# Optimization experiments

Measured on AMD Instinct MI355X. Metric: run time of the kernel, lower is better.

## Reference

```python
import jax, jax.numpy as jnp
import numpy as np

N_NODES = 50000
N_EDGES = 800000
HIDDEN = 64
RES = 0.5  # args.res_layer


def setup_inputs() -> dict:
    key = jax.random.key(0)
    ks = jax.random.split(key, 9)
    s = 0.05  # scale weights to keep exp(att) stable
    return {
        "edge_index": jax.random.randint(ks[0], (2, N_EDGES), 0, N_NODES, dtype=jnp.int32),
        "adj_values": jax.random.uniform(ks[1], (N_EDGES,), dtype=jnp.float32),
        "embeds": jax.random.normal(ks[2], (N_NODES, HIDDEN), dtype=jnp.float32),
        "W1": jax.random.normal(ks[3], (HIDDEN, HIDDEN), dtype=jnp.float32) * s,
        "b1": jax.random.normal(ks[4], (HIDDEN,), dtype=jnp.float32) * s,
        "W2": jax.random.normal(ks[5], (HIDDEN, HIDDEN), dtype=jnp.float32) * s,
        "b2": jax.random.normal(ks[6], (HIDDEN,), dtype=jnp.float32) * s,
        "att_w": jax.random.normal(ks[7], (2 * HIDDEN,), dtype=jnp.float32) * s,
        "att_b": jax.random.normal(ks[8], (1,), dtype=jnp.float32) * s,
    }


def reference(edge_index, adj_values, embeds, W1, b1, W2, b2, att_w, att_b):
    n = embeds.shape[0]
    h = embeds.shape[1]
    row, col = edge_index[0], edge_index[1]
    # per-edge gather + two small linears with ReLU
    f1 = jax.nn.relu(embeds[row] @ W1 + b1)          # [E, h]
    f2 = jax.nn.relu(embeds[col] @ W2 + b2)          # [E, h]
    # attention score = Linear(concat(f1, f2)) -> split weight, avoid concat
    att = f1 @ att_w[:h] + f2 @ att_w[h:] + att_b[0]  # [E]
    exp_att = jnp.exp(att)
    # sparse row-wise softmax denominator via segment sum
    rowsum = jax.ops.segment_sum(exp_att, row, num_segments=n) + 1e-6  # [N]
    values = (exp_att / rowsum[row] + RES * adj_values) / (1.0 + RES)  # [E]
    # SpMM: out[i] = sum_{e: row[e]=i} values[e] * embeds[col[e]]
    out = jax.ops.segment_sum(values[:, None] * embeds[col], row, num_segments=n)  # [N, h]
    return values, out
```

## Files before the change

### kernel.cpp

```cpp
#include <hip/hip_runtime.h>
#include <hip/hip_bf16.h>

#define HID 64
#define RES_F 0.5f
#define SLOTS 64

typedef __attribute__((ext_vector_type(8))) short short8;
typedef __attribute__((ext_vector_type(4))) float f32x4;

__device__ __forceinline__ float lane_bcast_f(float v, int k) {
    return __builtin_bit_cast(float, __builtin_amdgcn_readlane(__builtin_bit_cast(int, v), k));
}
__device__ __forceinline__ int lane_bcast_i(int v, int k) {
    return __builtin_amdgcn_readlane(v, k);
}
__device__ __forceinline__ short f2bf(float x) {
    __hip_bfloat16 h = __float2bfloat16(x);
    return __builtin_bit_cast(short, h);
}

__global__ void __launch_bounds__(256) fused_prep_kernel(
    const float* __restrict__ embeds,
    const float* __restrict__ W1, const float* __restrict__ W2,
    const float* __restrict__ b1, const float* __restrict__ b2,
    const float* __restrict__ att_w,
    const int* __restrict__ row, const int* __restrict__ col,
    const float* __restrict__ adj,
    int* __restrict__ cursor, int4* __restrict__ edata,
    float* __restrict__ a1, float* __restrict__ a2,
    __hip_bfloat162* __restrict__ embeds_bf,
    int n, int E, int nodeBlocks, int edgeBlocks)
{
    __shared__ short sW[2 * HID * HID];

    if (blockIdx.x < nodeBlocks) {
        for (int i = threadIdx.x; i < HID * HID; i += blockDim.x) {
            sW[i]             = f2bf(W1[i]);
            sW[HID * HID + i] = f2bf(W2[i]);
        }
        __syncthreads();

        const int lane = threadIdx.x & 63;
        const int colx = lane & 15;
        const int quad = lane >> 4;

        short8 bfrag[8][2];
        float  sac[8], bc[8];
#pragma unroll
        for (int cb = 0; cb < 8; ++cb) {
            const int jp = cb * 16 + colx;
            const short* w = (jp < HID) ? (sW + jp) : (sW + HID * HID + jp - HID);
#pragma unroll
            for (int kh = 0; kh < 2; ++kh) {
                short8 f;
#pragma unroll
                for (int j = 0; j < 8; ++j) {
                    const int k = kh * 32 + quad * 8 + j;
                    f[j] = w[k * HID];
                }
                bfrag[cb][kh] = f;
            }
            sac[cb] = att_w[jp];
            bc[cb]  = (jp < HID) ? b1[jp] : b2[jp - HID];
        }

        int gwave = (blockIdx.x * blockDim.x + threadIdx.x) >> 6;
        const int nwave = (nodeBlocks * blockDim.x) >> 6;
        const int nbatch = (n + 15) >> 4;

        for (int b = gwave; b < nbatch; b += nwave) {
            const int base = b << 4;
            int mrow = base + colx;
            if (mrow >= n) mrow = n - 1;
            const float* ep = embeds + (size_t)mrow * HID;
            short8 afrag0, afrag1;
#pragma unroll
            for (int j = 0; j < 8; ++j) {
                afrag0[j] = f2bf(ep[quad * 8 + j]);
                afrag1[j] = f2bf(ep[32 + quad * 8 + j]);
            }

            float acc1[4] = {0.f, 0.f, 0.f, 0.f};
            float acc2[4] = {0.f, 0.f, 0.f, 0.f};
#pragma unroll
            for (int cb = 0; cb < 8; ++cb) {
                f32x4 C = {0.f, 0.f, 0.f, 0.f};
                C = __builtin_amdgcn_mfma_f32_16x16x32_bf16(afrag0, bfrag[cb][0], C, 0, 0, 0);
                C = __builtin_amdgcn_mfma_f32_16x16x32_bf16(afrag1, bfrag[cb][1], C, 0, 0, 0);
#pragma unroll
                for (int reg = 0; reg < 4; ++reg) {
                    const float v = fmaxf(C[reg] + bc[cb], 0.f) * sac[cb];
                    if (cb < 4) acc1[reg] += v; else acc2[reg] += v;
                }
            }
#pragma unroll
            for (int reg = 0; reg < 4; ++reg) {
#pragma unroll
                for (int off = 1; off < 16; off <<= 1) {
                    acc1[reg] += __shfl_xor(acc1[reg], off, 64);
                    acc2[reg] += __shfl_xor(acc2[reg], off, 64);
                }
            }
            if (colx == 0) {
#pragma unroll
                for (int reg = 0; reg < 4; ++reg) {
                    const int i = base + quad * 4 + reg;
                    if (i < n) { a1[i] = acc1[reg]; a2[i] = acc2[reg]; }
                }
            }
        }
    } else {
        const int tid = (blockIdx.x - nodeBlocks) * blockDim.x + threadIdx.x;
        const int ts  = edgeBlocks * blockDim.x;

        const float2* ef2 = (const float2*)embeds;
        const int npair = n * (HID / 2);
        for (int i = tid; i < npair; i += ts) {
            float2 f = ef2[i];
            __hip_bfloat162 h;
            h.x = __float2bfloat16(f.x);
            h.y = __float2bfloat16(f.y);
            embeds_bf[i] = h;
        }

        for (int e = tid; e < E; e += ts) {
            const int r  = row[e];
            const int c  = col[e];
            const float aj = adj[e];
            const int p  = atomicAdd(&cursor[r], 1);
            if (p < SLOTS)
                edata[(size_t)r * SLOTS + p] =
                    make_int4(c, __float_as_int(aj), e, 0);
        }
    }
}

__global__ void __launch_bounds__(256) spmm_kernel(
    const int* __restrict__ cursor, const int4* __restrict__ edata,
    const __hip_bfloat16* __restrict__ embeds_bf,
    const float* __restrict__ a1, const float* __restrict__ a2,
    const float* __restrict__ att_b,
    float* __restrict__ values, float* __restrict__ out, int n)
{
    const float ab  = att_b[0];
    const float inv = 1.0f / (1.0f + RES_F);
    const int lane = threadIdx.x & 63;
    int r = (blockIdx.x * blockDim.x + threadIdx.x) >> 6;
    const int nwave = (gridDim.x * blockDim.x) >> 6;

    for (; r < n; r += nwave) {
        const int deg = min(cursor[r], SLOTS);
        const float a1r = a1[r];
        float acc = 0.0f;

        const bool valid = lane < deg;
        int c = 0, e = 0;
        float ex = 0.0f, aj = 0.0f;
        if (valid) {
            const int4 ed = edata[(size_t)r * SLOTS + lane];
            c  = ed.x;
            aj = __int_as_float(ed.y);
            e  = ed.z;
            ex = __expf(a1r + a2[c] + ab);
        }
        float rs = ex;
#pragma unroll
        for (int off = 1; off < 64; off <<= 1)
            rs += __shfl_xor(rs, off, 64);
        float v = 0.0f;
        if (valid) {
            v = (ex / (rs + 1e-6f) + RES_F * aj) * inv;
            values[e] = v;
        }
        int j = 0;
        for (; j + 8 <= deg; j += 8) {
            const int   c0 = lane_bcast_i(c, j + 0);
            const int   c1 = lane_bcast_i(c, j + 1);
            const int   c2 = lane_bcast_i(c, j + 2);
            const int   c3 = lane_bcast_i(c, j + 3);
            const int   c4 = lane_bcast_i(c, j + 4);
            const int   c5 = lane_bcast_i(c, j + 5);
            const int   c6 = lane_bcast_i(c, j + 6);
            const int   c7 = lane_bcast_i(c, j + 7);
            const float b0 = __bfloat162float(embeds_bf[c0 * HID + lane]);
            const float b1 = __bfloat162float(embeds_bf[c1 * HID + lane]);
            const float b2 = __bfloat162float(embeds_bf[c2 * HID + lane]);
            const float b3 = __bfloat162float(embeds_bf[c3 * HID + lane]);
            const float b4 = __bfloat162float(embeds_bf[c4 * HID + lane]);
            const float b5 = __bfloat162float(embeds_bf[c5 * HID + lane]);
            const float b6 = __bfloat162float(embeds_bf[c6 * HID + lane]);
            const float b7 = __bfloat162float(embeds_bf[c7 * HID + lane]);
            acc = fmaf(lane_bcast_f(v, j + 0), b0, acc);
            acc = fmaf(lane_bcast_f(v, j + 1), b1, acc);
            acc = fmaf(lane_bcast_f(v, j + 2), b2, acc);
            acc = fmaf(lane_bcast_f(v, j + 3), b3, acc);
            acc = fmaf(lane_bcast_f(v, j + 4), b4, acc);
            acc = fmaf(lane_bcast_f(v, j + 5), b5, acc);
            acc = fmaf(lane_bcast_f(v, j + 6), b6, acc);
            acc = fmaf(lane_bcast_f(v, j + 7), b7, acc);
        }
        for (; j < deg; ++j) {
            const int   cj = lane_bcast_i(c, j);
            const float vj = lane_bcast_f(v, j);
            acc = fmaf(vj, __bfloat162float(embeds_bf[cj * HID + lane]), acc);
        }
        out[r * HID + lane] = acc;
    }
}

extern "C" void kernel_launch(void* const* d_in, const int* in_sizes, int n_in,
                              void* d_out, int out_size, void* d_ws, size_t ws_size,
                              hipStream_t stream)
{
    const int* edge_index = (const int*)d_in[0];
    const float* adj      = (const float*)d_in[1];
    const float* embeds   = (const float*)d_in[2];
    const float* W1       = (const float*)d_in[3];
    const float* b1       = (const float*)d_in[4];
    const float* W2       = (const float*)d_in[5];
    const float* b2       = (const float*)d_in[6];
    const float* att_w    = (const float*)d_in[7];
    const float* att_b    = (const float*)d_in[8];

    const int E = in_sizes[1];
    const int N = in_sizes[2] / HID;

    const int* row = edge_index;
    const int* col = edge_index + E;

    int4*  edata  = (int4*)d_ws;
    float* a1     = (float*)(edata + (size_t)N * SLOTS);
    float* a2     = a1 + N;
    int*   cursor = (int*)(a2 + N);
    __hip_bfloat16* embeds_bf = (__hip_bfloat16*)(cursor + N);

    float* values = (float*)d_out;
    float* out    = values + E;

    (void)hipMemsetAsync(cursor, 0, (size_t)N * sizeof(int), stream);

    const int nodeBlocks = 512;
    const int edgeBlocks = 3125;
    fused_prep_kernel<<<nodeBlocks + edgeBlocks, 256, 0, stream>>>(
        embeds, W1, W2, b1, b2, att_w, row, col, adj,
        cursor, edata, a1, a2, (__hip_bfloat162*)embeds_bf,
        N, E, nodeBlocks, edgeBlocks);

    spmm_kernel<<<12544, 256, 0, stream>>>(cursor, edata, embeds_bf,
                                           a1, a2, att_b, values, out, N);
}
```

Measured before the change: 165.9 us.

## Write edge values to slot layout and remap with separate kernel

The bucket entry shrinks from int4 to int2 by dropping the edge index. The SpMM kernel now writes attention values into a coalesced per-row slot buffer instead of scattering them by edge id. A new remap kernel uses a per-edge recorded slot position to gather the values back into edge order. This replaces scattered writes with coalesced ones, at the cost of an extra kernel launch, an extra pos array write and read, and a gather read of the slot buffer.

```diff
diff --git a/kernel.cpp b/kernel.cpp
--- a/kernel.cpp
+++ b/kernel.cpp
@@ -26,7 +26,8 @@
     const float* __restrict__ att_w,
     const int* __restrict__ row, const int* __restrict__ col,
     const float* __restrict__ adj,
-    int* __restrict__ cursor, int4* __restrict__ edata,
+    int* __restrict__ cursor, int* __restrict__ pos,
+    int2* __restrict__ edata,
     float* __restrict__ a1, float* __restrict__ a2,
     __hip_bfloat162* __restrict__ embeds_bf,
     int n, int E, int nodeBlocks, int edgeBlocks)
@@ -127,20 +128,21 @@
             const int r  = row[e];
             const int c  = col[e];
             const float aj = adj[e];
-            const int p  = atomicAdd(&cursor[r], 1);
+            const int p = atomicAdd(&cursor[r], 1);
+            pos[e] = p;
             if (p < SLOTS)
                 edata[(size_t)r * SLOTS + p] =
-                    make_int4(c, __float_as_int(aj), e, 0);
+                    make_int2(c, __float_as_int(aj));
         }
     }
 }
 
 __global__ void __launch_bounds__(256) spmm_kernel(
-    const int* __restrict__ cursor, const int4* __restrict__ edata,
+    const int* __restrict__ cursor, const int2* __restrict__ edata,
     const __hip_bfloat16* __restrict__ embeds_bf,
     const float* __restrict__ a1, const float* __restrict__ a2,
     const float* __restrict__ att_b,
-    float* __restrict__ values, float* __restrict__ out, int n)
+    float* __restrict__ vslot, float* __restrict__ out, int n)
 {
     const float ab  = att_b[0];
     const float inv = 1.0f / (1.0f + RES_F);
@@ -154,13 +156,12 @@
         float acc = 0.0f;
 
         const bool valid = lane < deg;
-        int c = 0, e = 0;
+        int c = 0;
         float ex = 0.0f, aj = 0.0f;
         if (valid) {
-            const int4 ed = edata[(size_t)r * SLOTS + lane];
+            const int2 ed = edata[(size_t)r * SLOTS + lane];
             c  = ed.x;
             aj = __int_as_float(ed.y);
-            e  = ed.z;
             ex = __expf(a1r + a2[c] + ab);
         }
         float rs = ex;
@@ -170,7 +171,7 @@
         float v = 0.0f;
         if (valid) {
             v = (ex / (rs + 1e-6f) + RES_F * aj) * inv;
-            values[e] = v;
+            vslot[(size_t)r * SLOTS + lane] = v;
         }
         int j = 0;
         for (; j + 8 <= deg; j += 8) {
@@ -208,6 +209,20 @@
     }
 }
 
+__global__ void __launch_bounds__(256) remap_kernel(
+    const int* __restrict__ row, const int* __restrict__ pos,
+    const float* __restrict__ vslot,
+    float* __restrict__ values, int E)
+{
+    int e = blockIdx.x * blockDim.x + threadIdx.x;
+    const int stride = gridDim.x * blockDim.x;
+    for (; e < E; e += stride) {
+        const int r = row[e];
+        const int p = pos[e];
+        values[e] = (p < SLOTS) ? vslot[(size_t)r * SLOTS + p] : 0.0f;
+    }
+}
+
 extern "C" void kernel_launch(void* const* d_in, const int* in_sizes, int n_in,
                               void* d_out, int out_size, void* d_ws, size_t ws_size,
                               hipStream_t stream)
@@ -228,8 +243,10 @@
     const int* row = edge_index;
     const int* col = edge_index + E;
 
-    int4*  edata  = (int4*)d_ws;
-    float* a1     = (float*)(edata + (size_t)N * SLOTS);
+    int2*  edata  = (int2*)d_ws;
+    float* vslot  = (float*)(edata + (size_t)N * SLOTS);
+    int*   pos    = (int*)(vslot + (size_t)N * SLOTS);
+    float* a1     = (float*)(pos + E);
     float* a2     = a1 + N;
     int*   cursor = (int*)(a2 + N);
     __hip_bfloat16* embeds_bf = (__hip_bfloat16*)(cursor + N);
@@ -243,9 +260,11 @@
     const int edgeBlocks = 3125;
     fused_prep_kernel<<<nodeBlocks + edgeBlocks, 256, 0, stream>>>(
         embeds, W1, W2, b1, b2, att_w, row, col, adj,
-        cursor, edata, a1, a2, (__hip_bfloat162*)embeds_bf,
+        cursor, pos, edata, a1, a2, (__hip_bfloat162*)embeds_bf,
         N, E, nodeBlocks, edgeBlocks);
 
     spmm_kernel<<<12544, 256, 0, stream>>>(cursor, edata, embeds_bf,
-                                           a1, a2, att_b, values, out, N);
-}
+                                           a1, a2, att_b, vslot, out, N);
+
+    remap_kernel<<<3125, 256, 0, stream>>>(row, pos, vslot, values, E);
+}
```

Result: no change. 168.9 us (+1.8%).
